# Optimization experiments

Hardware: AMD Instinct MI355X
Metric: run time of the kernel (lower is better)

The kernel has to match this reference:

```python
import jax, jax.numpy as jnp
import numpy as np

B, N, TOKEN_DIM, HIDDEN = 4, 2048, 512, 128
LN_EPS = 1e-5
NEG_SLOPE = 0.01  # torch LeakyReLU default


def setup_inputs() -> dict:
    key = jax.random.key(0)
    ks = jax.random.split(key, 6)
    s_fc = 1.0 / np.sqrt(TOKEN_DIM)
    s_at = 1.0 / np.sqrt(2 * HIDDEN)
    return {
        "token_embedding": jax.random.normal(ks[0], (B, N, TOKEN_DIM), jnp.float32),
        "fc_w": jax.random.uniform(ks[1], (HIDDEN, TOKEN_DIM), jnp.float32, -s_fc, s_fc),
        "fc_b": jax.random.uniform(ks[2], (HIDDEN,), jnp.float32, -s_fc, s_fc),
        "attn_w": jax.random.uniform(ks[3], (1, 2 * HIDDEN), jnp.float32, -s_at, s_at),
        "attn_b": jax.random.uniform(ks[4], (1,), jnp.float32, -s_at, s_at),
        "ln_g": jnp.ones((HIDDEN,), jnp.float32),
        "ln_b": jnp.zeros((HIDDEN,), jnp.float32),
    }


def reference(token_embedding, fc_w, fc_b, attn_w, attn_b, ln_g, ln_b):
    # h = LayerNorm(Linear(x))  -> [B, N, H]
    h = jnp.einsum("bnt,ht->bnh", token_embedding, fc_w) + fc_b
    mu = jnp.mean(h, axis=-1, keepdims=True)
    var = jnp.mean(jnp.square(h - mu), axis=-1, keepdims=True)
    h = ln_g * (h - mu) * jax.lax.rsqrt(var + LN_EPS) + ln_b

    # Original: concat_h[b,i,j] = [h[b,j], h[b,i]] then attn_fc (dropout is identity at eval).
    # Algebraically: score[b,i,j] = h[b,j].w_row + h[b,i].w_col + bias
    w_row = attn_w[0, :HIDDEN]
    w_col = attn_w[0, HIDDEN:]
    s_row = h @ w_row  # [B, N]
    s_col = h @ w_col  # [B, N]
    e = s_col[:, :, None] + s_row[:, None, :] + attn_b[0]  # [B, N, N]
    e = jnp.where(e >= 0, e, NEG_SLOPE * e)  # LeakyReLU
    a = jax.nn.softmax(e, axis=-1)
    h_prime = jnp.einsum("bij,bjh->bih", a, h)
    return h_prime
```

## Files before the change

### kernel.cpp

```cpp
#include <hip/hip_runtime.h>

#define NB      4
#define NTOK    2048
#define TOKDIM  512
#define HID     128
#define NROWS   (NB * NTOK)
#define LN_EPS  1e-5f
#define NEG_SLOPE 0.01f

typedef short bf16x8 __attribute__((ext_vector_type(8)));
typedef float f32x4  __attribute__((ext_vector_type(4)));

static __device__ __forceinline__ unsigned short f2bf(float f) {
    union { float f; unsigned int i; } v; v.f = f;
    unsigned int i = v.i;
    i += 0x7FFFu + ((i >> 16) & 1u);
    return (unsigned short)(i >> 16);
}

__global__ __launch_bounds__(256) void k_prep(const float* __restrict__ W,
                                              unsigned short* __restrict__ Wb) {
    const int g = blockIdx.x * 256 + threadIdx.x;
    float4 v = *(const float4*)(W + (size_t)g * 4);
    ushort4 o;
    o.x = f2bf(v.x); o.y = f2bf(v.y); o.z = f2bf(v.z); o.w = f2bf(v.w);
    *(ushort4*)(Wb + (size_t)g * 4) = o;
}

__global__ __launch_bounds__(1024) void k_fused(const float* __restrict__ X,
                                                const unsigned short* __restrict__ Wb,
                                                const float* __restrict__ fcb,
                                                const float* __restrict__ attnw,
                                                const float* __restrict__ attnb,
                                                const float* __restrict__ lng,
                                                const float* __restrict__ lnb,
                                                unsigned short* __restrict__ hT,
                                                float* __restrict__ srow,
                                                float* __restrict__ cc) {
    __shared__ char smem[33280 + 32 * 132 * 4];
    unsigned short* ldsX = (unsigned short*)smem;
    unsigned short* ldsT = (unsigned short*)smem;
    float* hfull = (float*)(smem + 33280);

    const int tid   = threadIdx.x;
    const int wv    = tid >> 6;
    const int lane  = tid & 63;
    const int m     = lane & 15;
    const int q     = lane >> 4;
    const int rowbase = blockIdx.x * 32;
    const int nbase   = (wv & 7) * 16;
    const int rhalf   = (wv >> 3) * 16;

    {
        const int r  = tid >> 5;
        const int c0 = (tid & 31) * 16;
        const float* xp = X + (size_t)(rowbase + r) * TOKDIM + c0;
        bf16x8 v0, v1;
#pragma unroll
        for (int u = 0; u < 8; ++u) v0[u] = (short)f2bf(xp[u]);
#pragma unroll
        for (int u = 0; u < 8; ++u) v1[u] = (short)f2bf(xp[8 + u]);
        *(bf16x8*)&ldsX[r * 520 + c0]     = v0;
        *(bf16x8*)&ldsX[r * 520 + c0 + 8] = v1;
    }
    __syncthreads();

    const unsigned short* wp = Wb + (size_t)(nbase + m) * TOKDIM + q * 8;
    f32x4 acc = {0.f, 0.f, 0.f, 0.f};
#pragma unroll
    for (int kk = 0; kk < TOKDIM / 32; ++kk) {
        bf16x8 a = *(const bf16x8*)&ldsX[(rhalf + m) * 520 + kk * 32 + q * 8];
        bf16x8 b = *(const bf16x8*)(wp + kk * 32);
        acc = __builtin_amdgcn_mfma_f32_16x16x32_bf16(a, b, acc, 0, 0, 0);
    }

    {
        const float bias = fcb[nbase + m];
#pragma unroll
        for (int r = 0; r < 4; ++r)
            hfull[(rhalf + q * 4 + r) * 132 + nbase + m] = acc[r] + bias;
    }
    __syncthreads();

    {
        const int r   = tid >> 5;
        const int l32 = tid & 31;
        const int c0  = l32 * 4;
        float4 hv = *(const float4*)&hfull[r * 132 + c0];
        float v[4] = {hv.x, hv.y, hv.z, hv.w};

        float s  = v[0] + v[1] + v[2] + v[3];
        float ss = v[0]*v[0] + v[1]*v[1] + v[2]*v[2] + v[3]*v[3];
#pragma unroll
        for (int d = 1; d < 32; d <<= 1) {
            s  += __shfl_xor(s,  d, 64);
            ss += __shfl_xor(ss, d, 64);
        }
        float mu  = s * (1.f / HID);
        float var = ss * (1.f / HID) - mu * mu;
        float rs  = rsqrtf(var + LN_EPS);

        float n[4], sr = 0.f, sc = 0.f;
#pragma unroll
        for (int k = 0; k < 4; ++k) {
            n[k] = lng[c0 + k] * (v[k] - mu) * rs + lnb[c0 + k];
            sr += n[k] * attnw[c0 + k];
            sc += n[k] * attnw[HID + c0 + k];
            ldsT[(c0 + k) * 36 + r] = f2bf(n[k]);
        }
#pragma unroll
        for (int d = 1; d < 32; d <<= 1) {
            sr += __shfl_xor(sr, d, 64);
            sc += __shfl_xor(sc, d, 64);
        }
        if (l32 == 0) {
            int grow = rowbase + r;
            srow[grow] = sr;
            cc[grow]   = sc + attnb[0];
        }
    }
    __syncthreads();

    {
        const int d  = tid >> 3;
        const int j4 = (tid & 7) * 4;
        const int b    = blockIdx.x >> 6;
        const int jblk = (blockIdx.x & 63) * 32;
        ushort4 o;
        o.x = ldsT[d * 36 + j4 + 0];
        o.y = ldsT[d * 36 + j4 + 1];
        o.z = ldsT[d * 36 + j4 + 2];
        o.w = ldsT[d * 36 + j4 + 3];
        *(ushort4*)(hT + ((size_t)(b * HID + d)) * NTOK + jblk + j4) = o;
    }
}

static __device__ __forceinline__ void produce_chunk(
        unsigned short* __restrict__ dst,
        float ci, float4 s0, float4 s1, float4 s2, float4 s3,
        float& lsum) {
    float sv[16] = {s0.x, s0.y, s0.z, s0.w, s1.x, s1.y, s1.z, s1.w,
                    s2.x, s2.y, s2.z, s2.w, s3.x, s3.y, s3.z, s3.w};
    bf16x8 v0, v1;
#pragma unroll
    for (int u = 0; u < 8; ++u) {
        float z = ci + sv[u];
        z = fmaxf(z, NEG_SLOPE * z);
        float p = __expf(z);
        lsum += p;
        v0[u] = (short)f2bf(p);
    }
#pragma unroll
    for (int u = 0; u < 8; ++u) {
        float z = ci + sv[8 + u];
        z = fmaxf(z, NEG_SLOPE * z);
        float p = __expf(z);
        lsum += p;
        v1[u] = (short)f2bf(p);
    }
    *(bf16x8*)dst       = v0;
    *(bf16x8*)(dst + 8) = v1;
}

__global__ __launch_bounds__(512) void k_attn(const unsigned short* __restrict__ hT,
                                              const float* __restrict__ srow,
                                              const float* __restrict__ cc,
                                              float* __restrict__ out) {
    __shared__ unsigned short pP[2][32][264];
    __shared__ float pDen[32][16];
    __shared__ float denv[32];

    const int tid  = threadIdx.x;
    const int wv   = tid >> 6;
    const int lane = tid & 63;
    const int m    = lane & 15;
    const int q    = lane >> 4;
    const int rowbase = blockIdx.x * 32;
    const int b    = blockIdx.x >> 6;
    const int dbase = wv * 16;

    const int i_loc = tid >> 4;
    const int jseg  = (tid & 15) * 16;
    const float ci  = cc[rowbase + i_loc];
    const float* sp = srow + (size_t)b * NTOK + jseg;

    const unsigned short* hp =
        hT + ((size_t)(b * HID + dbase + m)) * NTOK + q * 8;

    f32x4 acc0 = {0.f, 0.f, 0.f, 0.f};
    f32x4 acc1 = {0.f, 0.f, 0.f, 0.f};
    float lsum = 0.f;

    float4 s0 = *(const float4*)(sp);
    float4 s1 = *(const float4*)(sp + 4);
    float4 s2 = *(const float4*)(sp + 8);
    float4 s3 = *(const float4*)(sp + 12);
    bf16x8 bcur[8], bnxt[8];
#pragma unroll
    for (int s = 0; s < 8; ++s) bcur[s] = *(const bf16x8*)(hp + s * 32);

    produce_chunk(&pP[0][i_loc][jseg], ci, s0, s1, s2, s3, lsum);

    float4 n0, n1, n2, n3;
    {
        const float* spn = sp + 256;
        n0 = *(const float4*)(spn);
        n1 = *(const float4*)(spn + 4);
        n2 = *(const float4*)(spn + 8);
        n3 = *(const float4*)(spn + 12);
    }

    __syncthreads();

#pragma unroll
    for (int ch = 0; ch < 8; ++ch) {
        if (ch < 7) {
            produce_chunk(&pP[(ch + 1) & 1][i_loc][jseg], ci, n0, n1, n2, n3, lsum);

            if (ch < 6) {
                const float* spn = sp + (ch + 2) * 256;
                n0 = *(const float4*)(spn);
                n1 = *(const float4*)(spn + 4);
                n2 = *(const float4*)(spn + 8);
                n3 = *(const float4*)(spn + 12);
            }
            const unsigned short* hpn = hp + (ch + 1) * 256;
#pragma unroll
            for (int s = 0; s < 8; ++s) bnxt[s] = *(const bf16x8*)(hpn + s * 32);
        }

#pragma unroll
        for (int s = 0; s < 8; ++s) {
            bf16x8 a0 = *(const bf16x8*)&pP[ch & 1][m][s * 32 + q * 8];
            bf16x8 a1 = *(const bf16x8*)&pP[ch & 1][16 + m][s * 32 + q * 8];
            acc0 = __builtin_amdgcn_mfma_f32_16x16x32_bf16(a0, bcur[s], acc0, 0, 0, 0);
            acc1 = __builtin_amdgcn_mfma_f32_16x16x32_bf16(a1, bcur[s], acc1, 0, 0, 0);
        }

        __syncthreads();

#pragma unroll
        for (int s = 0; s < 8; ++s) bcur[s] = bnxt[s];
    }

    pDen[i_loc][tid & 15] = lsum;
    __syncthreads();
    if (tid < 32) {
        float d = 0.f;
#pragma unroll
        for (int k = 0; k < 16; ++k) d += pDen[tid][k];
        denv[tid] = 1.f / d;
    }
    __syncthreads();

#pragma unroll
    for (int r = 0; r < 4; ++r) {
        int r0 = q * 4 + r;
        out[(size_t)(rowbase + r0) * HID + dbase + m]      = acc0[r] * denv[r0];
        out[(size_t)(rowbase + 16 + r0) * HID + dbase + m] = acc1[r] * denv[16 + r0];
    }
}

extern "C" void kernel_launch(void* const* d_in, const int* in_sizes, int n_in,
                              void* d_out, int out_size, void* d_ws, size_t ws_size,
                              hipStream_t stream) {
    const float* X     = (const float*)d_in[0];
    const float* W     = (const float*)d_in[1];
    const float* fcb   = (const float*)d_in[2];
    const float* attnw = (const float*)d_in[3];
    const float* attnb = (const float*)d_in[4];
    const float* lng   = (const float*)d_in[5];
    const float* lnb   = (const float*)d_in[6];
    float* out = (float*)d_out;

    char* ws = (char*)d_ws;
    unsigned short* hT   = (unsigned short*)ws;
    float*          srow = (float*)(ws + 2u * 1024 * 1024);
    float*          cchd = (float*)(ws + 2u * 1024 * 1024 + 32u * 1024);
    unsigned short* Wb   = (unsigned short*)(ws + 2u * 1024 * 1024 + 64u * 1024);

    k_prep <<<64, 256, 0, stream>>>(W, Wb);
    k_fused<<<NROWS / 32, 1024, 0, stream>>>(X, Wb, fcb, attnw, attnb, lng, lnb,
                                             hT, srow, cchd);
    k_attn <<<NROWS / 32, 512, 0, stream>>>(hT, srow, cchd, out);
}
```

Measured before the change: 105.6 us.

## Split attention K dimension across wave pairs with 32x32 register tiles

Each wave now computes a 32-row by 32-column output tile over half of each 256-wide j chunk, instead of a 32x16 tile over the full chunk. Every A fragment loaded from shared memory is reused for two MFMAs and every B fragment for two, which halves the LDS A reads per MFMA and the global B loads per wave. The two K-halves are reduced through a new shared-memory buffer at the end, adding about 17KB of LDS and an extra sync.

```diff
diff --git a/kernel.cpp b/kernel.cpp
--- a/kernel.cpp
+++ b/kernel.cpp
@@ -167,6 +167,7 @@
                                               const float* __restrict__ cc,
                                               float* __restrict__ out) {
     __shared__ unsigned short pP[2][32][264];
+    __shared__ float pC[32][132];
     __shared__ float pDen[32][16];
     __shared__ float denv[32];
 
@@ -177,27 +178,36 @@
     const int q    = lane >> 4;
     const int rowbase = blockIdx.x * 32;
     const int b    = blockIdx.x >> 6;
-    const int dbase = wv * 16;
+
+    const int dgrp = (wv & 3) * 32;
+    const int h    = wv >> 2;
+    const int hk   = h * 128;
 
     const int i_loc = tid >> 4;
     const int jseg  = (tid & 15) * 16;
     const float ci  = cc[rowbase + i_loc];
     const float* sp = srow + (size_t)b * NTOK + jseg;
 
-    const unsigned short* hp =
-        hT + ((size_t)(b * HID + dbase + m)) * NTOK + q * 8;
-
-    f32x4 acc0 = {0.f, 0.f, 0.f, 0.f};
-    f32x4 acc1 = {0.f, 0.f, 0.f, 0.f};
+    const unsigned short* hp0 =
+        hT + ((size_t)(b * HID + dgrp + m)) * NTOK + hk + q * 8;
+    const unsigned short* hp1 = hp0 + 16 * NTOK;
+
+    f32x4 acc00 = {0.f, 0.f, 0.f, 0.f};
+    f32x4 acc01 = {0.f, 0.f, 0.f, 0.f};
+    f32x4 acc10 = {0.f, 0.f, 0.f, 0.f};
+    f32x4 acc11 = {0.f, 0.f, 0.f, 0.f};
     float lsum = 0.f;
 
     float4 s0 = *(const float4*)(sp);
     float4 s1 = *(const float4*)(sp + 4);
     float4 s2 = *(const float4*)(sp + 8);
     float4 s3 = *(const float4*)(sp + 12);
-    bf16x8 bcur[8], bnxt[8];
-#pragma unroll
-    for (int s = 0; s < 8; ++s) bcur[s] = *(const bf16x8*)(hp + s * 32);
+    bf16x8 bc0[4], bc1[4], bn0[4], bn1[4];
+#pragma unroll
+    for (int s = 0; s < 4; ++s) {
+        bc0[s] = *(const bf16x8*)(hp0 + s * 32);
+        bc1[s] = *(const bf16x8*)(hp1 + s * 32);
+    }
 
     produce_chunk(&pP[0][i_loc][jseg], ci, s0, s1, s2, s3, lsum);
 
@@ -224,23 +234,31 @@
                 n2 = *(const float4*)(spn + 8);
                 n3 = *(const float4*)(spn + 12);
             }
-            const unsigned short* hpn = hp + (ch + 1) * 256;
-#pragma unroll
-            for (int s = 0; s < 8; ++s) bnxt[s] = *(const bf16x8*)(hpn + s * 32);
-        }
-
-#pragma unroll
-        for (int s = 0; s < 8; ++s) {
-            bf16x8 a0 = *(const bf16x8*)&pP[ch & 1][m][s * 32 + q * 8];
-            bf16x8 a1 = *(const bf16x8*)&pP[ch & 1][16 + m][s * 32 + q * 8];
-            acc0 = __builtin_amdgcn_mfma_f32_16x16x32_bf16(a0, bcur[s], acc0, 0, 0, 0);
-            acc1 = __builtin_amdgcn_mfma_f32_16x16x32_bf16(a1, bcur[s], acc1, 0, 0, 0);
+            const unsigned short* g0 = hp0 + (ch + 1) * 256;
+            const unsigned short* g1 = hp1 + (ch + 1) * 256;
+#pragma unroll
+            for (int s = 0; s < 4; ++s) {
+                bn0[s] = *(const bf16x8*)(g0 + s * 32);
+                bn1[s] = *(const bf16x8*)(g1 + s * 32);
+            }
+        }
+
+#pragma unroll
+        for (int s = 0; s < 4; ++s) {
+            bf16x8 a0 = *(const bf16x8*)&pP[ch & 1][m][hk + s * 32 + q * 8];
+            bf16x8 a1 = *(const bf16x8*)&pP[ch & 1][16 + m][hk + s * 32 + q * 8];
+            acc00 = __builtin_amdgcn_mfma_f32_16x16x32_bf16(a0, bc0[s], acc00, 0, 0, 0);
+            acc01 = __builtin_amdgcn_mfma_f32_16x16x32_bf16(a0, bc1[s], acc01, 0, 0, 0);
+            acc10 = __builtin_amdgcn_mfma_f32_16x16x32_bf16(a1, bc0[s], acc10, 0, 0, 0);
+            acc11 = __builtin_amdgcn_mfma_f32_16x16x32_bf16(a1, bc1[s], acc11, 0, 0, 0);
         }
 
         __syncthreads();
 
-#pragma unroll
-        for (int s = 0; s < 8; ++s) bcur[s] = bnxt[s];
+        if (ch < 7) {
+#pragma unroll
+            for (int s = 0; s < 4; ++s) { bc0[s] = bn0[s]; bc1[s] = bn1[s]; }
+        }
     }
 
     pDen[i_loc][tid & 15] = lsum;
@@ -251,13 +269,29 @@
         for (int k = 0; k < 16; ++k) d += pDen[tid][k];
         denv[tid] = 1.f / d;
     }
-    __syncthreads();
-
-#pragma unroll
-    for (int r = 0; r < 4; ++r) {
-        int r0 = q * 4 + r;
-        out[(size_t)(rowbase + r0) * HID + dbase + m]      = acc0[r] * denv[r0];
-        out[(size_t)(rowbase + 16 + r0) * HID + dbase + m] = acc1[r] * denv[16 + r0];
+    if (h == 0) {
+#pragma unroll
+        for (int r = 0; r < 4; ++r) {
+            pC[q * 4 + r][dgrp + m]           = acc00[r];
+            pC[q * 4 + r][dgrp + 16 + m]      = acc01[r];
+            pC[16 + q * 4 + r][dgrp + m]      = acc10[r];
+            pC[16 + q * 4 + r][dgrp + 16 + m] = acc11[r];
+        }
+    }
+    __syncthreads();
+    if (h == 1) {
+#pragma unroll
+        for (int r = 0; r < 4; ++r) {
+            int r0 = q * 4 + r;
+            float v00 = (pC[r0][dgrp + m]           + acc00[r]) * denv[r0];
+            float v01 = (pC[r0][dgrp + 16 + m]      + acc01[r]) * denv[r0];
+            float v10 = (pC[16 + r0][dgrp + m]      + acc10[r]) * denv[16 + r0];
+            float v11 = (pC[16 + r0][dgrp + 16 + m] + acc11[r]) * denv[16 + r0];
+            out[(size_t)(rowbase + r0) * HID + dgrp + m]           = v00;
+            out[(size_t)(rowbase + r0) * HID + dgrp + 16 + m]      = v01;
+            out[(size_t)(rowbase + 16 + r0) * HID + dgrp + m]      = v10;
+            out[(size_t)(rowbase + 16 + r0) * HID + dgrp + 16 + m] = v11;
+        }
     }
 }
 
```

After: 107.0 us. Within noise of the previous version (+1.3%).

## Warp-specialize attention kernel into producer and MFMA consumer waves

Applied to the files above, without the earlier changes.

Splits the 8 waves of k_attn into 4 producer waves that compute exp/LeakyReLU probabilities into LDS and 4 consumer waves that run the MFMA accumulation. Each consumer wave now covers 32 hidden dims with a 2x2 accumulator tile instead of 16, so each A fragment read from LDS feeds two MFMAs. The B-operand loads are split into half-chunk prefetches. The aim is to overlap exp work with matrix math and cut LDS traffic, at the cost of leaving half the waves idle during each phase and raising per-wave register pressure.

```diff
diff --git a/kernel.cpp b/kernel.cpp
--- a/kernel.cpp
+++ b/kernel.cpp
@@ -135,39 +135,12 @@
     }
 }
 
-static __device__ __forceinline__ void produce_chunk(
-        unsigned short* __restrict__ dst,
-        float ci, float4 s0, float4 s1, float4 s2, float4 s3,
-        float& lsum) {
-    float sv[16] = {s0.x, s0.y, s0.z, s0.w, s1.x, s1.y, s1.z, s1.w,
-                    s2.x, s2.y, s2.z, s2.w, s3.x, s3.y, s3.z, s3.w};
-    bf16x8 v0, v1;
-#pragma unroll
-    for (int u = 0; u < 8; ++u) {
-        float z = ci + sv[u];
-        z = fmaxf(z, NEG_SLOPE * z);
-        float p = __expf(z);
-        lsum += p;
-        v0[u] = (short)f2bf(p);
-    }
-#pragma unroll
-    for (int u = 0; u < 8; ++u) {
-        float z = ci + sv[8 + u];
-        z = fmaxf(z, NEG_SLOPE * z);
-        float p = __expf(z);
-        lsum += p;
-        v1[u] = (short)f2bf(p);
-    }
-    *(bf16x8*)dst       = v0;
-    *(bf16x8*)(dst + 8) = v1;
-}
-
 __global__ __launch_bounds__(512) void k_attn(const unsigned short* __restrict__ hT,
                                               const float* __restrict__ srow,
                                               const float* __restrict__ cc,
                                               float* __restrict__ out) {
     __shared__ unsigned short pP[2][32][264];
-    __shared__ float pDen[32][16];
+    __shared__ float pDen[32][8];
     __shared__ float denv[32];
 
     const int tid  = threadIdx.x;
@@ -177,87 +150,129 @@
     const int q    = lane >> 4;
     const int rowbase = blockIdx.x * 32;
     const int b    = blockIdx.x >> 6;
-    const int dbase = wv * 16;
-
-    const int i_loc = tid >> 4;
-    const int jseg  = (tid & 15) * 16;
-    const float ci  = cc[rowbase + i_loc];
-    const float* sp = srow + (size_t)b * NTOK + jseg;
-
-    const unsigned short* hp =
-        hT + ((size_t)(b * HID + dbase + m)) * NTOK + q * 8;
-
-    f32x4 acc0 = {0.f, 0.f, 0.f, 0.f};
-    f32x4 acc1 = {0.f, 0.f, 0.f, 0.f};
+    const bool producer = (wv < 4);
+
+    const int i_loc = tid >> 3;
+    const int jsub  = (tid & 7) * 32;
+    float ci = 0.f;
+    const float* sp = srow + (size_t)b * NTOK + jsub;
     float lsum = 0.f;
-
-    float4 s0 = *(const float4*)(sp);
-    float4 s1 = *(const float4*)(sp + 4);
-    float4 s2 = *(const float4*)(sp + 8);
-    float4 s3 = *(const float4*)(sp + 12);
-    bf16x8 bcur[8], bnxt[8];
-#pragma unroll
-    for (int s = 0; s < 8; ++s) bcur[s] = *(const bf16x8*)(hp + s * 32);
-
-    produce_chunk(&pP[0][i_loc][jseg], ci, s0, s1, s2, s3, lsum);
-
-    float4 n0, n1, n2, n3;
-    {
-        const float* spn = sp + 256;
-        n0 = *(const float4*)(spn);
-        n1 = *(const float4*)(spn + 4);
-        n2 = *(const float4*)(spn + 8);
-        n3 = *(const float4*)(spn + 12);
-    }
-
+    float4 nxt[8];
+
+    const int cw   = wv - 4;
+    const int dgrp = cw * 32;
+    const unsigned short* hp0 =
+        hT + ((size_t)(b * HID + dgrp + m)) * NTOK + q * 8;
+    const unsigned short* hp1 = hp0 + 16 * NTOK;
+    f32x4 acc00 = {0.f, 0.f, 0.f, 0.f};
+    f32x4 acc01 = {0.f, 0.f, 0.f, 0.f};
+    f32x4 acc10 = {0.f, 0.f, 0.f, 0.f};
+    f32x4 acc11 = {0.f, 0.f, 0.f, 0.f};
+    bf16x8 bA0[4], bA1[4], bB0[4], bB1[4];
+
+#define PRODUCE32(buf, F)                                                       \
+    {                                                                           \
+        unsigned short* dst = &pP[buf][i_loc][jsub];                            \
+        _Pragma("unroll")                                                       \
+        for (int g = 0; g < 4; ++g) {                                           \
+            float e[8] = {F[2*g].x, F[2*g].y, F[2*g].z, F[2*g].w,               \
+                          F[2*g+1].x, F[2*g+1].y, F[2*g+1].z, F[2*g+1].w};      \
+            bf16x8 w;                                                           \
+            _Pragma("unroll")                                                   \
+            for (int u = 0; u < 8; ++u) {                                       \
+                float z = ci + e[u];                                            \
+                z = fmaxf(z, NEG_SLOPE * z);                                    \
+                float p = __expf(z);                                            \
+                lsum += p;                                                      \
+                w[u] = (short)f2bf(p);                                          \
+            }                                                                   \
+            *(bf16x8*)(dst + g * 8) = w;                                        \
+        }                                                                       \
+    }
+
+    if (producer) {
+        ci = cc[rowbase + i_loc];
+        float4 cur[8];
+#pragma unroll
+        for (int g = 0; g < 8; ++g) cur[g] = *(const float4*)(sp + g * 4);
+        PRODUCE32(0, cur)
+#pragma unroll
+        for (int g = 0; g < 8; ++g) nxt[g] = *(const float4*)(sp + 256 + g * 4);
+    } else {
+#pragma unroll
+        for (int s = 0; s < 4; ++s) {
+            bA0[s] = *(const bf16x8*)(hp0 + s * 32);
+            bA1[s] = *(const bf16x8*)(hp1 + s * 32);
+        }
+    }
     __syncthreads();
 
 #pragma unroll
     for (int ch = 0; ch < 8; ++ch) {
-        if (ch < 7) {
-            produce_chunk(&pP[(ch + 1) & 1][i_loc][jseg], ci, n0, n1, n2, n3, lsum);
-
-            if (ch < 6) {
-                const float* spn = sp + (ch + 2) * 256;
-                n0 = *(const float4*)(spn);
-                n1 = *(const float4*)(spn + 4);
-                n2 = *(const float4*)(spn + 8);
-                n3 = *(const float4*)(spn + 12);
-            }
-            const unsigned short* hpn = hp + (ch + 1) * 256;
-#pragma unroll
-            for (int s = 0; s < 8; ++s) bnxt[s] = *(const bf16x8*)(hpn + s * 32);
-        }
-
-#pragma unroll
-        for (int s = 0; s < 8; ++s) {
-            bf16x8 a0 = *(const bf16x8*)&pP[ch & 1][m][s * 32 + q * 8];
-            bf16x8 a1 = *(const bf16x8*)&pP[ch & 1][16 + m][s * 32 + q * 8];
-            acc0 = __builtin_amdgcn_mfma_f32_16x16x32_bf16(a0, bcur[s], acc0, 0, 0, 0);
-            acc1 = __builtin_amdgcn_mfma_f32_16x16x32_bf16(a1, bcur[s], acc1, 0, 0, 0);
-        }
-
+        if (producer) {
+            if (ch < 7) {
+                PRODUCE32((ch + 1) & 1, nxt)
+                if (ch < 6) {
+                    const float* spn = sp + (ch + 2) * 256;
+#pragma unroll
+                    for (int g = 0; g < 8; ++g) nxt[g] = *(const float4*)(spn + g * 4);
+                }
+            } else {
+                pDen[i_loc][tid & 7] = lsum;
+            }
+        } else {
+#pragma unroll
+            for (int s = 0; s < 4; ++s) {
+                bB0[s] = *(const bf16x8*)(hp0 + ch * 256 + 128 + s * 32);
+                bB1[s] = *(const bf16x8*)(hp1 + ch * 256 + 128 + s * 32);
+            }
+#pragma unroll
+            for (int s = 0; s < 4; ++s) {
+                bf16x8 a0 = *(const bf16x8*)&pP[ch & 1][m][s * 32 + q * 8];
+                bf16x8 a1 = *(const bf16x8*)&pP[ch & 1][16 + m][s * 32 + q * 8];
+                acc00 = __builtin_amdgcn_mfma_f32_16x16x32_bf16(a0, bA0[s], acc00, 0, 0, 0);
+                acc01 = __builtin_amdgcn_mfma_f32_16x16x32_bf16(a0, bA1[s], acc01, 0, 0, 0);
+                acc10 = __builtin_amdgcn_mfma_f32_16x16x32_bf16(a1, bA0[s], acc10, 0, 0, 0);
+                acc11 = __builtin_amdgcn_mfma_f32_16x16x32_bf16(a1, bA1[s], acc11, 0, 0, 0);
+            }
+            if (ch < 7) {
+#pragma unroll
+                for (int s = 0; s < 4; ++s) {
+                    bA0[s] = *(const bf16x8*)(hp0 + (ch + 1) * 256 + s * 32);
+                    bA1[s] = *(const bf16x8*)(hp1 + (ch + 1) * 256 + s * 32);
+                }
+            }
+#pragma unroll
+            for (int s = 0; s < 4; ++s) {
+                bf16x8 a0 = *(const bf16x8*)&pP[ch & 1][m][128 + s * 32 + q * 8];
+                bf16x8 a1 = *(const bf16x8*)&pP[ch & 1][16 + m][128 + s * 32 + q * 8];
+                acc00 = __builtin_amdgcn_mfma_f32_16x16x32_bf16(a0, bB0[s], acc00, 0, 0, 0);
+                acc01 = __builtin_amdgcn_mfma_f32_16x16x32_bf16(a0, bB1[s], acc01, 0, 0, 0);
+                acc10 = __builtin_amdgcn_mfma_f32_16x16x32_bf16(a1, bB0[s], acc10, 0, 0, 0);
+                acc11 = __builtin_amdgcn_mfma_f32_16x16x32_bf16(a1, bB1[s], acc11, 0, 0, 0);
+            }
+        }
         __syncthreads();
-
-#pragma unroll
-        for (int s = 0; s < 8; ++s) bcur[s] = bnxt[s];
-    }
-
-    pDen[i_loc][tid & 15] = lsum;
-    __syncthreads();
+    }
+#undef PRODUCE32
+
     if (tid < 32) {
         float d = 0.f;
 #pragma unroll
-        for (int k = 0; k < 16; ++k) d += pDen[tid][k];
+        for (int k = 0; k < 8; ++k) d += pDen[tid][k];
         denv[tid] = 1.f / d;
     }
     __syncthreads();
 
-#pragma unroll
-    for (int r = 0; r < 4; ++r) {
-        int r0 = q * 4 + r;
-        out[(size_t)(rowbase + r0) * HID + dbase + m]      = acc0[r] * denv[r0];
-        out[(size_t)(rowbase + 16 + r0) * HID + dbase + m] = acc1[r] * denv[16 + r0];
+    if (!producer) {
+#pragma unroll
+        for (int r = 0; r < 4; ++r) {
+            int r0 = q * 4 + r;
+            out[(size_t)(rowbase + r0) * HID + dgrp + m]           = acc00[r] * denv[r0];
+            out[(size_t)(rowbase + r0) * HID + dgrp + 16 + m]      = acc01[r] * denv[r0];
+            out[(size_t)(rowbase + 16 + r0) * HID + dgrp + m]      = acc10[r] * denv[16 + r0];
+            out[(size_t)(rowbase + 16 + r0) * HID + dgrp + 16 + m] = acc11[r] * denv[16 + r0];
+        }
     }
 }
 
```

Measured after the change: 110.1 us. 1.04x slower.

## Replace quadratic attention with binned sort and prefix-sum softmax decomposition

Applied to the files above, without the earlier changes.

Because each score is c_i + s_j, the LeakyReLU branch depends only on whether s_j >= -c_i. The softmax then splits into exp(c_i)·exp(s_j) terms on one side of that threshold and exp(0.01c_i)·exp(0.01s_j) terms on the other. The change buckets s_j into histogram bins, builds suffix and prefix sums of the weighted h rows, and reads each output row from those tables at the threshold index. This removes the O(N²) exp and MFMA work. In exchange it adds several small, serial, low-occupancy kernels, gathered loads and roughly 8 MB of scan tables, and elements sharing the threshold's bin can land on the wrong branch, which introduces a small approximation.

```diff
diff --git a/kernel.cpp b/kernel.cpp
--- a/kernel.cpp
+++ b/kernel.cpp
@@ -7,6 +7,8 @@
 #define NROWS   (NB * NTOK)
 #define LN_EPS  1e-5f
 #define NEG_SLOPE 0.01f
+#define NBIN    1024
+#define TBSTR   (2049 * 128)
 
 typedef short bf16x8 __attribute__((ext_vector_type(8)));
 typedef float f32x4  __attribute__((ext_vector_type(4)));
@@ -34,12 +36,11 @@
                                                 const float* __restrict__ attnb,
                                                 const float* __restrict__ lng,
                                                 const float* __restrict__ lnb,
-                                                unsigned short* __restrict__ hT,
+                                                float* __restrict__ hOut,
                                                 float* __restrict__ srow,
                                                 float* __restrict__ cc) {
     __shared__ char smem[33280 + 32 * 132 * 4];
     unsigned short* ldsX = (unsigned short*)smem;
-    unsigned short* ldsT = (unsigned short*)smem;
     float* hfull = (float*)(smem + 33280);
 
     const int tid   = threadIdx.x;
@@ -100,14 +101,15 @@
         float var = ss * (1.f / HID) - mu * mu;
         float rs  = rsqrtf(var + LN_EPS);
 
-        float n[4], sr = 0.f, sc = 0.f;
+        float n0[4], sr = 0.f, sc = 0.f;
 #pragma unroll
         for (int k = 0; k < 4; ++k) {
-            n[k] = lng[c0 + k] * (v[k] - mu) * rs + lnb[c0 + k];
-            sr += n[k] * attnw[c0 + k];
-            sc += n[k] * attnw[HID + c0 + k];
-            ldsT[(c0 + k) * 36 + r] = f2bf(n[k]);
-        }
+            n0[k] = lng[c0 + k] * (v[k] - mu) * rs + lnb[c0 + k];
+            sr += n0[k] * attnw[c0 + k];
+            sc += n0[k] * attnw[HID + c0 + k];
+        }
+        float4 ho = {n0[0], n0[1], n0[2], n0[3]};
+        *(float4*)&hOut[(size_t)(rowbase + r) * HID + c0] = ho;
 #pragma unroll
         for (int d = 1; d < 32; d <<= 1) {
             sr += __shfl_xor(sr, d, 64);
@@ -119,145 +121,214 @@
             cc[grow]   = sc + attnb[0];
         }
     }
-    __syncthreads();
-
-    {
-        const int d  = tid >> 3;
-        const int j4 = (tid & 7) * 4;
-        const int b    = blockIdx.x >> 6;
-        const int jblk = (blockIdx.x & 63) * 32;
-        ushort4 o;
-        o.x = ldsT[d * 36 + j4 + 0];
-        o.y = ldsT[d * 36 + j4 + 1];
-        o.z = ldsT[d * 36 + j4 + 2];
-        o.w = ldsT[d * 36 + j4 + 3];
-        *(ushort4*)(hT + ((size_t)(b * HID + d)) * NTOK + jblk + j4) = o;
-    }
-}
-
-static __device__ __forceinline__ void produce_chunk(
-        unsigned short* __restrict__ dst,
-        float ci, float4 s0, float4 s1, float4 s2, float4 s3,
-        float& lsum) {
-    float sv[16] = {s0.x, s0.y, s0.z, s0.w, s1.x, s1.y, s1.z, s1.w,
-                    s2.x, s2.y, s2.z, s2.w, s3.x, s3.y, s3.z, s3.w};
-    bf16x8 v0, v1;
-#pragma unroll
-    for (int u = 0; u < 8; ++u) {
-        float z = ci + sv[u];
-        z = fmaxf(z, NEG_SLOPE * z);
-        float p = __expf(z);
-        lsum += p;
-        v0[u] = (short)f2bf(p);
-    }
-#pragma unroll
-    for (int u = 0; u < 8; ++u) {
-        float z = ci + sv[8 + u];
-        z = fmaxf(z, NEG_SLOPE * z);
-        float p = __expf(z);
-        lsum += p;
-        v1[u] = (short)f2bf(p);
-    }
-    *(bf16x8*)dst       = v0;
-    *(bf16x8*)(dst + 8) = v1;
-}
-
-__global__ __launch_bounds__(512) void k_attn(const unsigned short* __restrict__ hT,
-                                              const float* __restrict__ srow,
-                                              const float* __restrict__ cc,
-                                              float* __restrict__ out) {
-    __shared__ unsigned short pP[2][32][264];
-    __shared__ float pDen[32][16];
-    __shared__ float denv[32];
-
-    const int tid  = threadIdx.x;
-    const int wv   = tid >> 6;
-    const int lane = tid & 63;
-    const int m    = lane & 15;
-    const int q    = lane >> 4;
-    const int rowbase = blockIdx.x * 32;
-    const int b    = blockIdx.x >> 6;
-    const int dbase = wv * 16;
-
-    const int i_loc = tid >> 4;
-    const int jseg  = (tid & 15) * 16;
-    const float ci  = cc[rowbase + i_loc];
-    const float* sp = srow + (size_t)b * NTOK + jseg;
-
-    const unsigned short* hp =
-        hT + ((size_t)(b * HID + dbase + m)) * NTOK + q * 8;
-
-    f32x4 acc0 = {0.f, 0.f, 0.f, 0.f};
-    f32x4 acc1 = {0.f, 0.f, 0.f, 0.f};
-    float lsum = 0.f;
-
-    float4 s0 = *(const float4*)(sp);
-    float4 s1 = *(const float4*)(sp + 4);
-    float4 s2 = *(const float4*)(sp + 8);
-    float4 s3 = *(const float4*)(sp + 12);
-    bf16x8 bcur[8], bnxt[8];
-#pragma unroll
-    for (int s = 0; s < 8; ++s) bcur[s] = *(const bf16x8*)(hp + s * 32);
-
-    produce_chunk(&pP[0][i_loc][jseg], ci, s0, s1, s2, s3, lsum);
-
-    float4 n0, n1, n2, n3;
-    {
-        const float* spn = sp + 256;
-        n0 = *(const float4*)(spn);
-        n1 = *(const float4*)(spn + 4);
-        n2 = *(const float4*)(spn + 8);
-        n3 = *(const float4*)(spn + 12);
-    }
-
-    __syncthreads();
-
-#pragma unroll
-    for (int ch = 0; ch < 8; ++ch) {
-        if (ch < 7) {
-            produce_chunk(&pP[(ch + 1) & 1][i_loc][jseg], ci, n0, n1, n2, n3, lsum);
-
-            if (ch < 6) {
-                const float* spn = sp + (ch + 2) * 256;
-                n0 = *(const float4*)(spn);
-                n1 = *(const float4*)(spn + 4);
-                n2 = *(const float4*)(spn + 8);
-                n3 = *(const float4*)(spn + 12);
+}
+
+__global__ __launch_bounds__(1024) void k_sortscan(const float* __restrict__ srow,
+                                                   int* __restrict__ sIdx,
+                                                   float* __restrict__ E1s,
+                                                   float* __restrict__ E2s,
+                                                   int* __restrict__ binStart,
+                                                   float2* __restrict__ loscale) {
+    __shared__ int   hist[NBIN];
+    __shared__ int   cur[NBIN];
+    __shared__ int   bst[NBIN];
+    __shared__ int   chunkOff[32];
+    __shared__ float wmin[16], wmax[16];
+    __shared__ float sLo, sSc;
+
+    const int b   = blockIdx.x;
+    const int tid = threadIdx.x;
+    const float v0 = srow[b * NTOK + tid];
+    const float v1 = srow[b * NTOK + 1024 + tid];
+    hist[tid] = 0;
+
+    float mn = fminf(v0, v1), mx = fmaxf(v0, v1);
+#pragma unroll
+    for (int d = 1; d < 64; d <<= 1) {
+        mn = fminf(mn, __shfl_xor(mn, d, 64));
+        mx = fmaxf(mx, __shfl_xor(mx, d, 64));
+    }
+    if ((tid & 63) == 0) { wmin[tid >> 6] = mn; wmax[tid >> 6] = mx; }
+    __syncthreads();
+    if (tid == 0) {
+        float lo = wmin[0], hi = wmax[0];
+        for (int k = 1; k < 16; ++k) { lo = fminf(lo, wmin[k]); hi = fmaxf(hi, wmax[k]); }
+        float range = fmaxf(hi - lo, 1e-6f);
+        sLo = lo; sSc = (float)(NBIN - 1) / range;
+        float2 ls; ls.x = lo; ls.y = sSc;
+        loscale[b] = ls;
+    }
+    __syncthreads();
+    const float lo = sLo, scl = sSc;
+    int b0 = (int)((v0 - lo) * scl); b0 = b0 < 0 ? 0 : (b0 > NBIN - 1 ? NBIN - 1 : b0);
+    int b1 = (int)((v1 - lo) * scl); b1 = b1 < 0 ? 0 : (b1 > NBIN - 1 ? NBIN - 1 : b1);
+    atomicAdd(&hist[b0], 1);
+    atomicAdd(&hist[b1], 1);
+    __syncthreads();
+
+    if (tid < 32) {
+        int s = 0;
+        for (int m2 = 0; m2 < 32; ++m2) s += hist[tid * 32 + m2];
+        chunkOff[tid] = s;
+    }
+    __syncthreads();
+    if (tid == 0) {
+        int run = 0;
+        for (int c = 0; c < 32; ++c) { int t = chunkOff[c]; chunkOff[c] = run; run += t; }
+    }
+    __syncthreads();
+    {
+        int base = tid & ~31;
+        int off = chunkOff[tid >> 5];
+        for (int m2 = base; m2 < tid; ++m2) off += hist[m2];
+        bst[tid] = off;
+        cur[tid] = off;
+    }
+    __syncthreads();
+
+    {
+        int slot = atomicAdd(&cur[b0], 1);
+        sIdx[b * NTOK + slot] = tid;
+        E1s[b * NTOK + slot] = __expf(v0);
+        E2s[b * NTOK + slot] = __expf(NEG_SLOPE * v0);
+    }
+    {
+        int slot = atomicAdd(&cur[b1], 1);
+        sIdx[b * NTOK + slot] = 1024 + tid;
+        E1s[b * NTOK + slot] = __expf(v1);
+        E2s[b * NTOK + slot] = __expf(NEG_SLOPE * v1);
+    }
+    binStart[b * (NBIN + 1) + tid] = bst[tid];
+    if (tid == 0) binStart[b * (NBIN + 1) + NBIN] = NTOK;
+}
+
+__global__ __launch_bounds__(512) void k_scan(const float* __restrict__ h,
+                                              const int* __restrict__ sIdx,
+                                              const float* __restrict__ E1s,
+                                              const float* __restrict__ E2s,
+                                              float* __restrict__ SS1,
+                                              float* __restrict__ PS2,
+                                              float* __restrict__ ss1s,
+                                              float* __restrict__ ps2s) {
+    __shared__ float part1[32][128], part2[32][128];
+    __shared__ float off1[32][128], off2[32][128];
+    __shared__ float sp1[32], sp2[32];
+
+    const int bid = blockIdx.x;
+    const int tid = threadIdx.x;
+
+    if (bid < 32) {
+        const int b = bid >> 3, seg = bid & 7;
+        const int d = tid & 127, q = tid >> 7;
+        const int*   si = sIdx + b * NTOK;
+        const float* e1 = E1s + b * NTOK;
+        const float* e2 = E2s + b * NTOK;
+        const float* hb = h + (size_t)b * NTOK * HID;
+
+        for (int sub = q * 8; sub < q * 8 + 8; ++sub) {
+            float a1 = 0.f, a2 = 0.f;
+            for (int kk = 0; kk < 64; ++kk) {
+                int k = sub * 64 + kk;
+                float hv = hb[(size_t)si[k] * HID + d];
+                a1 += e1[k] * hv;
+                a2 += e2[k] * hv;
             }
-            const unsigned short* hpn = hp + (ch + 1) * 256;
-#pragma unroll
-            for (int s = 0; s < 8; ++s) bnxt[s] = *(const bf16x8*)(hpn + s * 32);
-        }
-
-#pragma unroll
-        for (int s = 0; s < 8; ++s) {
-            bf16x8 a0 = *(const bf16x8*)&pP[ch & 1][m][s * 32 + q * 8];
-            bf16x8 a1 = *(const bf16x8*)&pP[ch & 1][16 + m][s * 32 + q * 8];
-            acc0 = __builtin_amdgcn_mfma_f32_16x16x32_bf16(a0, bcur[s], acc0, 0, 0, 0);
-            acc1 = __builtin_amdgcn_mfma_f32_16x16x32_bf16(a1, bcur[s], acc1, 0, 0, 0);
-        }
-
+            part1[sub][d] = a1;
+            part2[sub][d] = a2;
+        }
         __syncthreads();
-
-#pragma unroll
-        for (int s = 0; s < 8; ++s) bcur[s] = bnxt[s];
-    }
-
-    pDen[i_loc][tid & 15] = lsum;
-    __syncthreads();
-    if (tid < 32) {
-        float d = 0.f;
-#pragma unroll
-        for (int k = 0; k < 16; ++k) d += pDen[tid][k];
-        denv[tid] = 1.f / d;
-    }
-    __syncthreads();
-
-#pragma unroll
-    for (int r = 0; r < 4; ++r) {
-        int r0 = q * 4 + r;
-        out[(size_t)(rowbase + r0) * HID + dbase + m]      = acc0[r] * denv[r0];
-        out[(size_t)(rowbase + 16 + r0) * HID + dbase + m] = acc1[r] * denv[16 + r0];
+        if (q == 0) {
+            float r2 = 0.f;
+            for (int s = 0; s < 32; ++s) { off2[s][d] = r2; r2 += part2[s][d]; }
+            float r1 = 0.f;
+            for (int s = 31; s >= 0; --s) { off1[s][d] = r1; r1 += part1[s][d]; }
+        }
+        __syncthreads();
+
+        const int sub = seg * 4 + q;
+        float* S = SS1 + (size_t)b * TBSTR;
+        float* P = PS2 + (size_t)b * TBSTR;
+        float run2 = off2[sub][d];
+        for (int kk = 0; kk < 64; ++kk) {
+            int k = sub * 64 + kk;
+            float hv = hb[(size_t)si[k] * HID + d];
+            P[(size_t)k * HID + d] = run2;
+            run2 += e2[k] * hv;
+        }
+        if (sub == 31) {
+            P[(size_t)NTOK * HID + d] = run2;
+            S[(size_t)NTOK * HID + d] = 0.f;
+        }
+        float run1 = off1[sub][d];
+        for (int kk = 63; kk >= 0; --kk) {
+            int k = sub * 64 + kk;
+            float hv = hb[(size_t)si[k] * HID + d];
+            run1 += e1[k] * hv;
+            S[(size_t)k * HID + d] = run1;
+        }
+    } else {
+        const int b = bid - 32;
+        const float* e1 = E1s + b * NTOK;
+        const float* e2 = E2s + b * NTOK;
+        if (tid < 32) {
+            float a1 = 0.f, a2 = 0.f;
+            for (int kk = 0; kk < 64; ++kk) { a1 += e1[tid * 64 + kk]; a2 += e2[tid * 64 + kk]; }
+            sp1[tid] = a1; sp2[tid] = a2;
+        }
+        __syncthreads();
+        if (tid < 32) {
+            float o2 = 0.f; for (int s = 0; s < tid; ++s)      o2 += sp2[s];
+            float o1 = 0.f; for (int s = tid + 1; s < 32; ++s) o1 += sp1[s];
+            float* pb = ps2s + b * 2049;
+            float* sb = ss1s + b * 2049;
+            float run2 = o2;
+            for (int kk = 0; kk < 64; ++kk) { int k = tid * 64 + kk; pb[k] = run2; run2 += e2[k]; }
+            if (tid == 31) { pb[NTOK] = run2; sb[NTOK] = 0.f; }
+            float run1 = o1;
+            for (int kk = 63; kk >= 0; --kk) { int k = tid * 64 + kk; run1 += e1[k]; sb[k] = run1; }
+        }
+    }
+}
+
+__global__ __launch_bounds__(512) void k_out(const float* __restrict__ cc,
+                                             const int* __restrict__ binStart,
+                                             const float2* __restrict__ loscale,
+                                             const float* __restrict__ SS1,
+                                             const float* __restrict__ PS2,
+                                             const float* __restrict__ ss1s,
+                                             const float* __restrict__ ps2s,
+                                             float* __restrict__ out) {
+    const int bid = blockIdx.x;
+    const int b = bid >> 5, rb = bid & 31;
+    const int tid = threadIdx.x;
+    const int rl = tid >> 3, oct = tid & 7;
+    const int grow = b * NTOK + rb * 64 + rl;
+
+    const float ci  = cc[grow];
+    const float2 ls = loscale[b];
+    const float e1i = __expf(ci);
+    const float e2i = __expf(NEG_SLOPE * ci);
+    const float fi  = (-ci - ls.x) * ls.y;
+    int r;
+    if (fi < 0.f)             r = 0;
+    else if (fi >= (float)NBIN) r = NTOK;
+    else                      r = binStart[b * (NBIN + 1) + (int)fi + 1];
+
+    const float den  = e1i * ss1s[b * 2049 + r] + e2i * ps2s[b * 2049 + r];
+    const float rden = 1.f / den;
+    const float* S = SS1 + (size_t)b * TBSTR + (size_t)r * HID + oct * 16;
+    const float* P = PS2 + (size_t)b * TBSTR + (size_t)r * HID + oct * 16;
+    float* o = out + (size_t)grow * HID + oct * 16;
+#pragma unroll
+    for (int g = 0; g < 4; ++g) {
+        float4 sv = *(const float4*)(S + g * 4);
+        float4 pv = *(const float4*)(P + g * 4);
+        float4 ov;
+        ov.x = (e1i * sv.x + e2i * pv.x) * rden;
+        ov.y = (e1i * sv.y + e2i * pv.y) * rden;
+        ov.z = (e1i * sv.z + e2i * pv.z) * rden;
+        ov.w = (e1i * sv.w + e2i * pv.w) * rden;
+        *(float4*)(o + g * 4) = ov;
     }
 }
 
@@ -274,13 +345,24 @@
     float* out = (float*)d_out;
 
     char* ws = (char*)d_ws;
-    unsigned short* hT   = (unsigned short*)ws;
-    float*          srow = (float*)(ws + 2u * 1024 * 1024);
-    float*          cchd = (float*)(ws + 2u * 1024 * 1024 + 32u * 1024);
-    unsigned short* Wb   = (unsigned short*)(ws + 2u * 1024 * 1024 + 64u * 1024);
-
-    k_prep <<<64, 256, 0, stream>>>(W, Wb);
-    k_fused<<<NROWS / 32, 1024, 0, stream>>>(X, Wb, fcb, attnw, attnb, lng, lnb,
-                                             hT, srow, cchd);
-    k_attn <<<NROWS / 32, 512, 0, stream>>>(hT, srow, cchd, out);
-}
+    float*          hO   = (float*)(ws);
+    float*          srow = (float*)(ws + 4194304);
+    float*          cchd = (float*)(ws + 4194304 + 32768);
+    unsigned short* Wb   = (unsigned short*)(ws + 4194304 + 65536);
+    int*            sIdx = (int*)(ws + 4194304 + 196608);
+    float*          E1s  = (float*)(ws + 4194304 + 229376);
+    float*          E2s  = (float*)(ws + 4194304 + 262144);
+    int*            binS = (int*)(ws + 4194304 + 294912);
+    float2*         losc = (float2*)(ws + 4194304 + 327680);
+    float*          SS1  = (float*)(ws + 8388608);
+    float*          PS2  = (float*)(ws + 12582912);
+    float*          ss1s = (float*)(ws + 17825792);
+    float*          ps2s = (float*)(ws + 17825792 + 65536);
+
+    k_prep    <<<64, 256, 0, stream>>>(W, Wb);
+    k_fused   <<<NROWS / 32, 1024, 0, stream>>>(X, Wb, fcb, attnw, attnb, lng, lnb,
+                                                hO, srow, cchd);
+    k_sortscan<<<NB, 1024, 0, stream>>>(srow, sIdx, E1s, E2s, binS, losc);
+    k_scan    <<<36, 512, 0, stream>>>(hO, sIdx, E1s, E2s, SS1, PS2, ss1s, ps2s);
+    k_out     <<<128, 512, 0, stream>>>(cchd, binS, losc, SS1, PS2, ss1s, ps2s, out);
+}
```

Result: slower. 152.4 us (+44.4%).
